# Kernel optimization log

Measured on AMD Instinct MI355X. Metric: run time of the kernel, lower is better.

## Reference

```python
import jax, jax.numpy as jnp
import numpy as np

LEVELS = 4
ATOMS_PER_LEVEL = [8, 16, 32, 64]   # [8] doubled per level
TOTAL_ATOMS = sum(ATOMS_PER_LEVEL)  # 120
KS = [2, 4, 8, 16]
CONNECTIVITY = 4


def _connection_matrices():
    # For each level i (except last), a [A_next, A_prev] count matrix C where
    # C[idx, j] += 1 for idx in [(2j + t) % A_next for t in range(4)].
    mats = []
    for i in range(LEVELS - 1):
        a_prev, a_next = ATOMS_PER_LEVEL[i], ATOMS_PER_LEVEL[i + 1]
        C = np.zeros((a_next, a_prev), dtype=np.float32)
        for j in range(a_prev):
            for t in range(j * 2, CONNECTIVITY + j * 2):
                C[t % a_next, j] += 1.0
        mats.append(jnp.asarray(C))
    return mats

CONN_MATS = _connection_matrices()


def _topk_keep(x, k):
    # Keep top-k by |value| along channel dim (axis=1), zero elsewhere.
    xt = jnp.moveaxis(x, 1, -1)              # [B,H,W,C]
    B, H, W, C = xt.shape
    xf = xt.reshape(-1, C)                   # [N,C]
    _, idx = jax.lax.top_k(jnp.abs(xf), k)   # [N,k]
    rows = jnp.arange(xf.shape[0])[:, None]
    mask = jnp.zeros(xf.shape, dtype=bool).at[rows, idx].set(True)
    out = jnp.where(mask, xf, jnp.zeros((), xf.dtype))
    return jnp.moveaxis(out.reshape(B, H, W, C), -1, 1)


def setup_inputs() -> dict:
    key = jax.random.key(0)
    kx, kw, kb = jax.random.split(key, 3)
    x = jax.random.normal(kx, (8, 3, 256, 256), dtype=jnp.float32)
    w = jax.random.normal(kw, (TOTAL_ATOMS, 3, 3, 3), dtype=jnp.float32) * 0.1
    b = jax.random.normal(kb, (TOTAL_ATOMS,), dtype=jnp.float32) * 0.01
    return {"x": x, "w": w, "b": b}


def reference(x, w, b):
    # Dictionary conv: 3x3, stride 1, VALID padding -> [B, 120, H-2, W-2]
    all_act = jax.lax.conv_general_dilated(
        x, w, window_strides=(1, 1), padding='VALID',
        dimension_numbers=('NCHW', 'OIHW', 'NCHW')) + b[None, :, None, None]

    outs = []
    descending_mask = None
    idx = 0
    for i, n_atoms in enumerate(ATOMS_PER_LEVEL):
        act = all_act[:, idx:idx + n_atoms]  # [B, A_i, H', W']
        idx += n_atoms
        if descending_mask is not None:
            # OR-gate: sum parent masks into connected child channels, threshold.
            gating = jnp.einsum('np,bphw->bnhw', CONN_MATS[i - 1], descending_mask)
            act = act * (gating > 0).astype(act.dtype)
        selected = _topk_keep(act, KS[i])
        descending_mask = (selected != 0).astype(act.dtype)
        outs.append(selected)
    return jnp.concatenate(outs, axis=1)
```

## Files before the change

### kernel.cpp

```cpp
#include <hip/hip_runtime.h>
#include <stdint.h>

static constexpr int HIN = 256, WIN = 256, HO = 254, WOUT = 254, NB = 8;
static constexpr int PLANE = HO * WOUT;
static constexpr int PIX = NB * PLANE;

typedef float f32x4 __attribute__((ext_vector_type(4)));

__device__ __align__(16) float g_wPad[4 * 27 * 64];
__device__ float g_bPad[4 * 64];

__constant__ int cN[4]   = {8, 16, 32, 64};
__constant__ int cK[4]   = {2, 4, 8, 16};
__constant__ int cCH0[4] = {0, 8, 24, 56};

__global__ void wprep(const float* __restrict__ w, const float* __restrict__ b) {
  int i = blockIdx.x * blockDim.x + threadIdx.x;
  if (i < 4 * 64) {
    int L = i / 64, j = i % 64;
    int N = 8 << L;
    int ch0 = (L == 0) ? 0 : (L == 1) ? 8 : (L == 2) ? 24 : 56;
    g_bPad[i] = (j < N) ? b[ch0 + j] : 0.0f;
  }
  if (i >= 4 * 27 * 64) return;
  int L = i / (27 * 64), r = i % (27 * 64), s = r / 64, j = r % 64;
  int N = 8 << L;
  int ch0 = (L == 0) ? 0 : (L == 1) ? 8 : (L == 2) ? 24 : 56;
  int ky = s / 9, kx = (s / 3) % 3, c = s % 3;
  g_wPad[i] = (j < N) ? w[(size_t)(ch0 + j) * 27 + c * 9 + ky * 3 + kx] : 0.0f;
}

__device__ __forceinline__ uint64_t spread_pairs(uint64_t mask, int a_next) {
  uint64_t s = mask;
  s = (s | (s << 16)) & 0x0000FFFF0000FFFFull;
  s = (s | (s << 8))  & 0x00FF00FF00FF00FFull;
  s = (s | (s << 4))  & 0x0F0F0F0F0F0F0F0Full;
  s = (s | (s << 2))  & 0x3333333333333333ull;
  s = (s | (s << 1))  & 0x5555555555555555ull;
  uint64_t pair = s | (s << 1);
  uint64_t lim = (a_next >= 64) ? ~0ull : ((1ull << a_next) - 1ull);
  uint64_t rot = ((pair << 2) | (pair >> (a_next - 2))) & lim;
  return (pair | rot) & lim;
}

__device__ __forceinline__ void bsort16(uint32_t (&v)[16]) {
#pragma unroll
  for (int sz = 2; sz <= 16; sz <<= 1) {
#pragma unroll
    for (int st = sz >> 1; st > 0; st >>= 1) {
#pragma unroll
      for (int i = 0; i < 16; ++i) {
        int l = i ^ st;
        if (l > i) {
          uint32_t a = v[i], c = v[l];
          uint32_t mx = a > c ? a : c;
          uint32_t mn = a > c ? c : a;
          bool desc = ((i & sz) == 0);
          v[i] = desc ? mx : mn;
          v[l] = desc ? mn : mx;
        }
      }
    }
  }
}

__device__ __forceinline__ void bmerge16(uint32_t (&v)[16]) {
#pragma unroll
  for (int st = 8; st > 0; st >>= 1) {
#pragma unroll
    for (int i = 0; i < 16; ++i) {
      int l = i ^ st;
      if (l > i) {
        uint32_t a = v[i], c = v[l];
        v[i] = a > c ? a : c;
        v[l] = a > c ? c : a;
      }
    }
  }
}

__global__ __launch_bounds__(128, 3)
void hrtk_main(const float* __restrict__ x, float* __restrict__ out) {
  __shared__ float smem[128 * 27];
  int p = blockIdx.x * blockDim.x + threadIdx.x;
  if (p >= PIX) return;
  int bi = p / PLANE;
  int r  = p % PLANE;
  int h  = r / WOUT;
  int wc = r % WOUT;

  float* pxl = &smem[threadIdx.x * 27];
  const float* xb = x + (size_t)bi * 3 * HIN * WIN;
#pragma unroll
  for (int ky = 0; ky < 3; ++ky)
#pragma unroll
    for (int kx = 0; kx < 3; ++kx)
#pragma unroll
      for (int c = 0; c < 3; ++c)
        pxl[ky * 9 + kx * 3 + c] =
            xb[c * HIN * WIN + (size_t)(h + ky) * WIN + (wc + kx)];

  uint32_t tofs4 = (uint32_t)(bi * 120 * PLANE + r) * 4u;
  char* outB = (char*)out;
  uint64_t allow = ~0ull;

#pragma unroll 1
  for (int lvl = 0; lvl < 4; ++lvl) {
    const int N = cN[lvl], K = cK[lvl], ch0 = cCH0[lvl];
    const float* wL = g_wPad + lvl * 27 * 64;
    const float* bL = g_bPad + lvl * 64;

    float act[64];
#pragma unroll
    for (int q = 0; q < 4; ++q)
      if (q * 16 < N) {
#pragma unroll
        for (int i = 0; i < 16; ++i) act[q * 16 + i] = 0.0f;
      }

#pragma unroll 1
    for (int g3 = 0; g3 < 3; ++g3) {
      const float* pg = pxl + g3 * 9;
      float pw[9];
#pragma unroll
      for (int ss = 0; ss < 9; ++ss) pw[ss] = pg[ss];
      const float* wg = wL + g3 * 9 * 64;
#pragma unroll
      for (int q = 0; q < 4; ++q)
        if (q * 16 < N) {
#pragma unroll
          for (int ss = 0; ss < 9; ++ss) {
            const f32x4* wr = (const f32x4*)(wg + ss * 64 + q * 16);
            f32x4 w0 = wr[0], w1 = wr[1], w2 = wr[2], w3 = wr[3];
#pragma unroll
            for (int i = 0; i < 4; ++i) {
              act[q * 16 + 0  + i] = __fmaf_rn(pw[ss], w0[i], act[q * 16 + 0  + i]);
              act[q * 16 + 4  + i] = __fmaf_rn(pw[ss], w1[i], act[q * 16 + 4  + i]);
              act[q * 16 + 8  + i] = __fmaf_rn(pw[ss], w2[i], act[q * 16 + 8  + i]);
              act[q * 16 + 12 + i] = __fmaf_rn(pw[ss], w3[i], act[q * 16 + 12 + i]);
            }
          }
        }
    }

#pragma unroll
    for (int q = 0; q < 4; ++q)
      if (q * 16 < N) {
#pragma unroll
        for (int i = 0; i < 16; ++i) {
          int j = q * 16 + i;
          float a = __fadd_rn(act[j], bL[j]);
          act[j] = ((allow >> j) & 1ull) ? a : 0.0f;
        }
      }

    uint32_t run[16];
#pragma unroll
    for (int i = 0; i < 16; ++i)
      run[i] = __float_as_uint(act[i]) & 0x7fffffffu;
    bsort16(run);
#pragma unroll
    for (int g = 1; g < 4; ++g) {
      if (g * 16 < N) {
        uint32_t tmp[16];
#pragma unroll
        for (int i = 0; i < 16; ++i)
          tmp[i] = __float_as_uint(act[g * 16 + i]) & 0x7fffffffu;
        bsort16(tmp);
#pragma unroll
        for (int i = 0; i < 16; ++i) {
          uint32_t c = tmp[15 - i];
          run[i] = run[i] > c ? run[i] : c;
        }
        bmerge16(run);
      }
    }

    uint32_t mb = 0;
#pragma unroll
    for (int i = 0; i < 16; ++i) mb = (i == K - 1) ? run[i] : mb;
    float m = __uint_as_float(mb);
    int quota = 0;
#pragma unroll
    for (int i = 0; i < 16; ++i) quota += (i < K && run[i] == mb) ? 1 : 0;

    uint64_t msk = 0;
#pragma unroll
    for (int q = 0; q < 4; ++q)
      if (q * 16 < N) {
#pragma unroll
        for (int i = 0; i < 16; ++i) {
          int j = q * 16 + i;
          float aj = fabsf(act[j]);
          bool eq = (aj == m);
          bool keep = (aj > m) || (eq && quota > 0);
          quota -= eq ? 1 : 0;
          float v = keep ? act[j] : 0.0f;
          *(float*)(outB + (size_t)(ch0 + j) * PLANE * 4 + tofs4) = v;
          msk |= (v != 0.0f) ? (1ull << j) : 0ull;
        }
      }

    if (lvl < 3) allow = spread_pairs(msk, cN[lvl + 1]);
  }
}

extern "C" void kernel_launch(void* const* d_in, const int* in_sizes, int n_in,
                              void* d_out, int out_size, void* d_ws, size_t ws_size,
                              hipStream_t stream) {
  const float* x = (const float*)d_in[0];
  const float* w = (const float*)d_in[1];
  const float* b = (const float*)d_in[2];
  float* out = (float*)d_out;

  wprep<<<dim3((4 * 27 * 64 + 255) / 256), dim3(256), 0, stream>>>(w, b);
  dim3 blk(128), grid((PIX + 127) / 128);
  hrtk_main<<<grid, blk, 0, stream>>>(x, out);
}
```

Before: 317.7 us.

## Stage output channels through shared memory for vectorized 16-byte stores

```diff
diff --git a/kernel.cpp b/kernel.cpp
--- a/kernel.cpp
+++ b/kernel.cpp
@@ -82,14 +82,16 @@
 __global__ __launch_bounds__(128, 3)
 void hrtk_main(const float* __restrict__ x, float* __restrict__ out) {
   __shared__ float smem[128 * 27];
-  int p = blockIdx.x * blockDim.x + threadIdx.x;
-  if (p >= PIX) return;
-  int bi = p / PLANE;
-  int r  = p % PLANE;
-  int h  = r / WOUT;
-  int wc = r % WOUT;
-
-  float* pxl = &smem[threadIdx.x * 27];
+  __shared__ float st[16][132];
+  int tid = threadIdx.x;
+  int bi  = blockIdx.y;
+  int r0  = blockIdx.x * 128;
+  int r   = r0 + tid;
+  int rr  = (r < PLANE) ? r : (PLANE - 1);
+  int h   = rr / WOUT;
+  int wc  = rr % WOUT;
+
+  float* pxl = &smem[tid * 27];
   const float* xb = x + (size_t)bi * 3 * HIN * WIN;
 #pragma unroll
   for (int ky = 0; ky < 3; ++ky)
@@ -100,7 +102,6 @@
         pxl[ky * 9 + kx * 3 + c] =
             xb[c * HIN * WIN + (size_t)(h + ky) * WIN + (wc + kx)];
 
-  uint32_t tofs4 = (uint32_t)(bi * 120 * PLANE + r) * 4u;
   char* outB = (char*)out;
   uint64_t allow = ~0ull;
 
@@ -185,20 +186,36 @@
     for (int i = 0; i < 16; ++i) quota += (i < K && run[i] == mb) ? 1 : 0;
 
     uint64_t msk = 0;
-#pragma unroll
-    for (int q = 0; q < 4; ++q)
-      if (q * 16 < N) {
+    const int npass = (N >= 16) ? 4 : 2;
+#pragma unroll
+    for (int q4 = 0; q4 < 4; ++q4)
+      if (q4 * 16 < N) {
 #pragma unroll
         for (int i = 0; i < 16; ++i) {
-          int j = q * 16 + i;
+          int j = q4 * 16 + i;
           float aj = fabsf(act[j]);
           bool eq = (aj == m);
           bool keep = (aj > m) || (eq && quota > 0);
           quota -= eq ? 1 : 0;
           float v = keep ? act[j] : 0.0f;
-          *(float*)(outB + (size_t)(ch0 + j) * PLANE * 4 + tofs4) = v;
+          st[i][tid] = v;
           msk |= (v != 0.0f) ? (1ull << j) : 0ull;
         }
+        __syncthreads();
+#pragma unroll
+        for (int ps = 0; ps < 4; ++ps) {
+          if (ps < npass) {
+            int ch = ps * 4 + (tid >> 5);
+            int qd = tid & 31;
+            int rq = r0 + qd * 4;
+            if (rq < PLANE) {
+              f32x4 vv = *(const f32x4*)&st[ch][qd * 4];
+              *(f32x4*)(outB +
+                  ((size_t)(bi * 120 + ch0 + q4 * 16 + ch) * PLANE + rq) * 4) = vv;
+            }
+          }
+        }
+        __syncthreads();
       }
 
     if (lvl < 3) allow = spread_pairs(msk, cN[lvl + 1]);
@@ -214,6 +231,6 @@
   float* out = (float*)d_out;
 
   wprep<<<dim3((4 * 27 * 64 + 255) / 256), dim3(256), 0, stream>>>(w, b);
-  dim3 blk(128), grid((PIX + 127) / 128);
+  dim3 blk(128), grid((PLANE + 127) / 128, NB);
   hrtk_main<<<grid, blk, 0, stream>>>(x, out);
 }
```

Result: slower. 469.2 us (+47.7%).
